# Performance work log

Measured on AMD Instinct MI355X. Metric: run time of the kernel, lower is better.

## Reference

```python
import jax, jax.numpy as jnp
import numpy as np

# dims: B batch, T seq, DM d_model, H kv heads, D head dim
B, T, DM = 4, 2048, 768
H, D = 4, 64          # n_kv_heads, d_head = d_model // n_heads = 768 // 12
DIM = H * D           # 256


def setup_inputs() -> dict:
    key = jax.random.key(0)
    kx, kq, kk, kv, ko, kg = jax.random.split(key, 6)
    s = 0.02  # init scale for weights
    return {
        "x": jax.random.normal(kx, (B, T, DM), jnp.float32),
        "Wq": jax.random.normal(kq, (DM, DIM), jnp.float32) * s,
        "Wk": jax.random.normal(kk, (DM, DIM), jnp.float32) * s,
        "Wv": jax.random.normal(kv, (DM, DIM), jnp.float32) * s,
        "Wo": jax.random.normal(ko, (DIM, DM), jnp.float32) * s,
        "Wg": jax.random.normal(kg, (DM, DM), jnp.float32) * s,
    }


def _feature_map(x):
    # F.elu(x) + 1.0  (strictly positive features)
    return jax.nn.elu(x) + 1.0


def reference(x, Wq, Wk, Wv, Wo, Wg):
    Bx, Tx, _ = x.shape
    q = _feature_map((x @ Wq).reshape(Bx, Tx, H, D))
    k = _feature_map((x @ Wk).reshape(Bx, Tx, H, D))
    v = (x @ Wv).reshape(Bx, Tx, H, D)

    # time-major for scan: [T, B, H, D]
    qT = q.transpose(1, 0, 2, 3)
    kT = k.transpose(1, 0, 2, 3)
    vT = v.transpose(1, 0, 2, 3)

    S0 = jnp.zeros((Bx, H, D, D), x.dtype)  # running sum of k v^T
    z0 = jnp.zeros((Bx, H, D), x.dtype)     # running sum of k

    def step(carry, inp):
        S, z = carry
        qi, ki, vi = inp  # each [B, H, D]
        S = S + ki[..., :, None] * vi[..., None, :]   # outer product update
        z = z + ki
        num = jnp.einsum('bhd,bhde->bhe', qi, S)
        den = jnp.maximum(jnp.sum(qi * z, axis=-1), 1e-6)  # clamp(min=1e-6)
        return (S, z), num / den[..., None]

    (_, _), outT = jax.lax.scan(step, (S0, z0), (qT, kT, vT))

    out = outT.transpose(1, 0, 2, 3).reshape(Bx, Tx, DIM)  # [B, T, H*D]
    gate = jax.nn.sigmoid(x @ Wg)
    return (out @ Wo) * gate
```

## Files before the change

kernel.cpp:

```cpp
#include <hip/hip_runtime.h>
#include <math.h>

typedef __attribute__((ext_vector_type(8))) short bf16x8;
typedef __attribute__((ext_vector_type(4))) float f32x4;

namespace {
constexpr int Bb  = 4;
constexpr int Tt  = 2048;
constexpr int DM  = 768;
constexpr int Hh  = 4;
constexpr int Dd  = 64;
constexpr int DIM = 256;
constexpr int BT  = Bb * Tt;
constexpr int CH  = 64;
constexpr int NC  = Tt / CH;
constexpr int NQKVG = 1536;
constexpr int MT  = BT / 128;
}

__device__ __forceinline__ float elu1(float x) { return x > 0.f ? x + 1.f : expf(x); }

__device__ __forceinline__ unsigned short f2bf(float f) {
  unsigned int x = __float_as_uint(f);
  unsigned int r = (x + 0x7fffu + ((x >> 16) & 1u)) >> 16;
  return (unsigned short)r;
}
__device__ __forceinline__ float bf2f(unsigned short u) {
  return __uint_as_float((unsigned int)u << 16);
}

__device__ __forceinline__ void gload16(const void* g, void* l) {
  __builtin_amdgcn_global_load_lds(
      (const __attribute__((address_space(1))) void*)g,
      (__attribute__((address_space(3))) void*)l, 16, 0, 0);
}

struct Stage32 {
  const short* a[2];
  const short* b[2];
  int seg;
  __device__ __forceinline__ void init(const short* Ag, size_t lda,
                                       const short* Bg, size_t ldb, int w, int l) {
    const int c16 = (l & 3) ^ ((l >> 3) & 3);
    seg = w * 2;
#pragma unroll
    for (int j = 0; j < 2; ++j) {
      int row = (seg + j) * 16 + (l >> 2);
      a[j] = Ag + (size_t)row * lda + c16 * 8;
      b[j] = Bg + (size_t)row * ldb + c16 * 8;
    }
  }
  __device__ __forceinline__ void issue(int k0, short* as, short* bs) const {
#pragma unroll
    for (int j = 0; j < 2; ++j) {
      gload16(a[j] + k0, (char*)as + (seg + j) * 1024);
      gload16(b[j] + k0, (char*)bs + (seg + j) * 1024);
    }
  }
};

__device__ __forceinline__ void xcd_tile(int bid, int& mt, int& nt) {
  int xcd = bid & 7;
  int idx = bid >> 3;
  mt = xcd * 8 + (idx & 7);
  nt = idx >> 3;
}

template <int NT>
__device__ __forceinline__ void kloop32(const Stage32& st, short* As0, short* As1,
                                        short* Bs0, short* Bs1,
                                        f32x4 (&acc)[4][4], int wr, int wc,
                                        int lr, int lg) {
  st.issue(0, As0, Bs0);
  st.issue(32, As1, Bs1);
#pragma unroll
  for (int t = 0; t < NT; ++t) {
    short* as = (t & 1) ? As1 : As0;
    short* bs = (t & 1) ? Bs1 : Bs0;
    if (t + 1 < NT)
      asm volatile("s_waitcnt vmcnt(4)" ::: "memory");
    else
      asm volatile("s_waitcnt vmcnt(0)" ::: "memory");
    __builtin_amdgcn_s_barrier();
    bf16x8 af[4], bf[4];
#pragma unroll
    for (int mi = 0; mi < 4; ++mi) {
      int r = wr * 64 + mi * 16 + lr;
      af[mi] = *(const bf16x8*)&as[r * 32 + (lg ^ ((r >> 1) & 3)) * 8];
    }
#pragma unroll
    for (int ni = 0; ni < 4; ++ni) {
      int r = wc * 64 + ni * 16 + lr;
      bf[ni] = *(const bf16x8*)&bs[r * 32 + (lg ^ ((r >> 1) & 3)) * 8];
    }
    asm volatile("s_waitcnt lgkmcnt(0)" ::: "memory");
    __builtin_amdgcn_sched_barrier(0);
    __builtin_amdgcn_s_barrier();
    if (t + 2 < NT) st.issue((t + 2) * 32, as, bs);
    __builtin_amdgcn_s_setprio(1);
#pragma unroll
    for (int mi = 0; mi < 4; ++mi)
#pragma unroll
      for (int ni = 0; ni < 4; ++ni)
        acc[mi][ni] = __builtin_amdgcn_mfma_f32_16x16x32_bf16(
            af[mi], bf[ni], acc[mi][ni], 0, 0, 0);
    __builtin_amdgcn_s_setprio(0);
  }
}

__global__ __launch_bounds__(256) void k_prep(
    const float* __restrict__ x, const float* __restrict__ Wq,
    const float* __restrict__ Wk, const float* __restrict__ Wv,
    const float* __restrict__ Wg, const float* __restrict__ Wo,
    unsigned short* __restrict__ xb, unsigned short* __restrict__ WT,
    unsigned short* __restrict__ WoT) {
  int bid = blockIdx.x;
  if (bid < 3072) {
    int i = bid * 256 + threadIdx.x;
    const float4* p = (const float4*)(x + (size_t)i * 8);
    float4 a = p[0], b = p[1];
    union { unsigned short u[8]; uint4 v; } r;
    r.u[0] = f2bf(a.x); r.u[1] = f2bf(a.y); r.u[2] = f2bf(a.z); r.u[3] = f2bf(a.w);
    r.u[4] = f2bf(b.x); r.u[5] = f2bf(b.y); r.u[6] = f2bf(b.z); r.u[7] = f2bf(b.w);
    *(uint4*)(xb + (size_t)i * 8) = r.v;
    return;
  }
  __shared__ float t[32][33];
  int idx = bid - 3072;
  const float* src;
  unsigned short* out;
  int K, N, n_off, ldo;
  if (idx < 576) {
    int z = idx / 192;
    idx %= 192;
    src = (z == 0) ? Wq : (z == 1) ? Wk : Wv;
    out = WT; K = 768; N = 256; n_off = z * 256; ldo = 768;
  } else if (idx < 1152) {
    idx -= 576;
    src = Wg; out = WT; K = 768; N = 768; n_off = 768; ldo = 768;
  } else {
    idx -= 1152;
    src = Wo; out = WoT; K = 256; N = 768; n_off = 0; ldo = 256;
  }
  int kt = idx % (K / 32), nt = idx / (K / 32);
  int k0 = kt * 32, n0 = nt * 32;
  const int tx = threadIdx.x & 31, ty = threadIdx.x >> 5;
  for (int i = ty; i < 32; i += 8)
    t[i][tx] = src[(size_t)(k0 + i) * N + n0 + tx];
  __syncthreads();
  for (int i = ty; i < 32; i += 8)
    out[(size_t)(n_off + n0 + i) * ldo + k0 + tx] = f2bf(t[tx][i]);
}

__global__ __launch_bounds__(256, 4) void k_gemm1(
    const unsigned short* __restrict__ xb, const unsigned short* __restrict__ WT,
    unsigned short* __restrict__ Q, unsigned short* __restrict__ K,
    unsigned short* __restrict__ V, unsigned short* __restrict__ G) {
  __shared__ __align__(16) char smem[32768];
  short* As0 = (short*)smem;
  short* As1 = (short*)(smem + 8192);
  short* Bs0 = (short*)(smem + 16384);
  short* Bs1 = (short*)(smem + 24576);
  const int tid = threadIdx.x;
  const int w = tid >> 6, l = tid & 63;
  const int lr = l & 15, lg = l >> 4;
  const int wr = w >> 1, wc = w & 1;
  int mt, nt;
  xcd_tile(blockIdx.x, mt, nt);
  const int m0 = mt * 128, n0 = nt * 128;

  Stage32 st;
  st.init((const short*)xb + (size_t)m0 * DM, DM,
          (const short*)WT + (size_t)n0 * DM, DM, w, l);

  f32x4 acc[4][4];
#pragma unroll
  for (int i = 0; i < 4; ++i)
#pragma unroll
    for (int j = 0; j < 4; ++j) acc[i][j] = (f32x4){0.f, 0.f, 0.f, 0.f};

  kloop32<DM / 32>(st, As0, As1, Bs0, Bs1, acc, wr, wc, lr, lg);
  __syncthreads();

  const int ttype = (n0 < 512) ? 0 : (n0 < 768) ? 1 : 2;
  unsigned short* Cs = (unsigned short*)smem;
#pragma unroll
  for (int mi = 0; mi < 4; ++mi)
#pragma unroll
    for (int ni = 0; ni < 4; ++ni)
#pragma unroll
      for (int r = 0; r < 4; ++r) {
        float v = acc[mi][ni][r];
        if (ttype == 0) v = elu1(v);
        else if (ttype == 2) v = 1.f / (1.f + expf(-v));
        Cs[(wr * 64 + mi * 16 + lg * 4 + r) * 128 + wc * 64 + ni * 16 + lr] =
            f2bf(v);
      }
  __syncthreads();
  unsigned short* dst;
  int ldd, cb;
  if (n0 < 256)      { dst = Q; ldd = DIM; cb = n0; }
  else if (n0 < 512) { dst = K; ldd = DIM; cb = n0 - 256; }
  else if (n0 < 768) { dst = V; ldd = DIM; cb = n0 - 512; }
  else               { dst = G; ldd = DM;  cb = n0 - 768; }
  const uint4* Cv = (const uint4*)Cs;
#pragma unroll
  for (int i = 0; i < 8; ++i) {
    int idx = tid + i * 256;
    int urow = idx >> 4, uc = idx & 15;
    *(uint4*)(dst + (size_t)(m0 + urow) * ldd + cb + uc * 8) = Cv[idx];
  }
}

__global__ __launch_bounds__(256) void k_chunksum(
    const unsigned short* __restrict__ K, const unsigned short* __restrict__ V,
    float* __restrict__ Sc, float* __restrict__ zc) {
  __shared__ float Ks[CH][68];
  __shared__ float Vs[CH][68];
  const int c = blockIdx.x, h = blockIdx.y, b = blockIdx.z;
  const int tx = threadIdx.x, ty = threadIdx.y;
  const int tid = ty * 16 + tx;
  const int t0 = c * CH;
#pragma unroll
  for (int l = 0; l < 4; ++l) {
    int idx = tid + l * 256;
    int d4 = idx & 15, t = idx >> 4;
    size_t o = (size_t)(b * Tt + t0 + t) * DIM + h * Dd + d4 * 4;
    short4 k4 = *(const short4*)(K + o);
    short4 v4 = *(const short4*)(V + o);
    Ks[t][d4 * 4 + 0] = bf2f(k4.x); Ks[t][d4 * 4 + 1] = bf2f(k4.y);
    Ks[t][d4 * 4 + 2] = bf2f(k4.z); Ks[t][d4 * 4 + 3] = bf2f(k4.w);
    Vs[t][d4 * 4 + 0] = bf2f(v4.x); Vs[t][d4 * 4 + 1] = bf2f(v4.y);
    Vs[t][d4 * 4 + 2] = bf2f(v4.z); Vs[t][d4 * 4 + 3] = bf2f(v4.w);
  }
  __syncthreads();
  float acc[4][4] = {};
  for (int t = 0; t < CH; ++t) {
    float4 k4 = *(const float4*)&Ks[t][ty * 4];
    float4 v4 = *(const float4*)&Vs[t][tx * 4];
    float kv[4] = {k4.x, k4.y, k4.z, k4.w};
    float vv[4] = {v4.x, v4.y, v4.z, v4.w};
#pragma unroll
    for (int i = 0; i < 4; ++i)
#pragma unroll
      for (int j = 0; j < 4; ++j) acc[i][j] += kv[i] * vv[j];
  }
  const size_t base = ((size_t)(b * Hh + h) * NC + c) * (Dd * Dd);
#pragma unroll
  for (int i = 0; i < 4; ++i) {
    float4 s4 = make_float4(acc[i][0], acc[i][1], acc[i][2], acc[i][3]);
    *(float4*)&Sc[base + (size_t)(ty * 4 + i) * Dd + tx * 4] = s4;
  }
  if (tid < Dd) {
    float s = 0.f;
    for (int t = 0; t < CH; ++t) s += Ks[t][tid];
    zc[((size_t)(b * Hh + h) * NC + c) * Dd + tid] = s;
  }
}

__global__ __launch_bounds__(256) void k_scan(float* __restrict__ Sc,
                                              float* __restrict__ zc) {
  const int bh = blockIdx.x;
  const int o = blockIdx.y * 256 + threadIdx.x;
  const size_t base = (size_t)bh * NC * (Dd * Dd) + o;
  float v[NC];
#pragma unroll
  for (int c = 0; c < NC; ++c) v[c] = Sc[base + (size_t)c * (Dd * Dd)];
  float run = 0.f;
#pragma unroll
  for (int c = 0; c < NC; ++c) {
    Sc[base + (size_t)c * (Dd * Dd)] = run;
    run += v[c];
  }
  if (blockIdx.y == 0 && threadIdx.x < Dd) {
    float rz = 0.f;
    for (int c = 0; c < NC; ++c) {
      size_t oz = ((size_t)bh * NC + c) * Dd + threadIdx.x;
      float cur = zc[oz];
      zc[oz] = rz;
      rz += cur;
    }
  }
}

__global__ __launch_bounds__(256) void k_out(
    const unsigned short* __restrict__ Q, const unsigned short* __restrict__ K,
    const unsigned short* __restrict__ V, const float* __restrict__ Sc,
    const float* __restrict__ zc, unsigned short* __restrict__ O) {
  __shared__ float Qs[CH][68];
  __shared__ float KVs[CH * 68];
  __shared__ float As[CH][68];
  __shared__ float Ss[Dd][68];
  __shared__ float zs[Dd];
  __shared__ float dens[CH];
  const int c = blockIdx.x, h = blockIdx.y, b = blockIdx.z;
  const int tx = threadIdx.x, ty = threadIdx.y;
  const int tid = ty * 16 + tx;
  const int t0 = c * CH;

#pragma unroll
  for (int l = 0; l < 4; ++l) {
    int idx = tid + l * 256;
    int d4 = idx & 15, t = idx >> 4;
    size_t o = (size_t)(b * Tt + t0 + t) * DIM + h * Dd + d4 * 4;
    short4 q4 = *(const short4*)(Q + o);
    short4 k4 = *(const short4*)(K + o);
    Qs[t][d4 * 4 + 0] = bf2f(q4.x); Qs[t][d4 * 4 + 1] = bf2f(q4.y);
    Qs[t][d4 * 4 + 2] = bf2f(q4.z); Qs[t][d4 * 4 + 3] = bf2f(q4.w);
    KVs[(d4 * 4 + 0) * 65 + t] = bf2f(k4.x);
    KVs[(d4 * 4 + 1) * 65 + t] = bf2f(k4.y);
    KVs[(d4 * 4 + 2) * 65 + t] = bf2f(k4.z);
    KVs[(d4 * 4 + 3) * 65 + t] = bf2f(k4.w);
  }
  __syncthreads();

  float acc[4][4] = {};
  for (int d0 = 0; d0 < Dd; d0 += 4) {
    float4 q4[4];
#pragma unroll
    for (int i = 0; i < 4; ++i) q4[i] = *(const float4*)&Qs[ty * 4 + i][d0];
#pragma unroll
    for (int dd = 0; dd < 4; ++dd) {
      int d = d0 + dd;
      float kv[4];
#pragma unroll
      for (int j = 0; j < 4; ++j) kv[j] = KVs[d * 65 + tx * 4 + j];
#pragma unroll
      for (int i = 0; i < 4; ++i) {
        float qv = ((const float*)&q4[i])[dd];
#pragma unroll
        for (int j = 0; j < 4; ++j) acc[i][j] += qv * kv[j];
      }
    }
  }
#pragma unroll
  for (int i = 0; i < 4; ++i)
#pragma unroll
    for (int j = 0; j < 4; ++j) {
      int ti = ty * 4 + i, sj = tx * 4 + j;
      As[ti][sj] = (sj <= ti) ? acc[i][j] : 0.f;
    }
  __syncthreads();

#pragma unroll
  for (int l = 0; l < 4; ++l) {
    int idx = tid + l * 256;
    int d4 = idx & 15, t = idx >> 4;
    size_t o = (size_t)(b * Tt + t0 + t) * DIM + h * Dd + d4 * 4;
    short4 v4 = *(const short4*)(V + o);
    KVs[t * 68 + d4 * 4 + 0] = bf2f(v4.x);
    KVs[t * 68 + d4 * 4 + 1] = bf2f(v4.y);
    KVs[t * 68 + d4 * 4 + 2] = bf2f(v4.z);
    KVs[t * 68 + d4 * 4 + 3] = bf2f(v4.w);
  }
  const size_t sbase = ((size_t)(b * Hh + h) * NC + c) * (Dd * Dd);
#pragma unroll
  for (int l = 0; l < 4; ++l) {
    int idx = tid + l * 256;
    int e4 = idx & 15, dd = idx >> 4;
    float4 s4 = *(const float4*)&Sc[sbase + (size_t)dd * Dd + e4 * 4];
    Ss[dd][e4 * 4 + 0] = s4.x; Ss[dd][e4 * 4 + 1] = s4.y;
    Ss[dd][e4 * 4 + 2] = s4.z; Ss[dd][e4 * 4 + 3] = s4.w;
  }
  if (tid < Dd) zs[tid] = zc[((size_t)(b * Hh + h) * NC + c) * Dd + tid];
  __syncthreads();

  if (tid < CH) {
    int i = tid;
    float rs = 0.f;
    for (int j = 0; j < CH; ++j) rs += As[i][j];
    float qz = 0.f;
    for (int d = 0; d < Dd; ++d) qz += Qs[i][d] * zs[d];
    dens[i] = fmaxf(rs + qz, 1e-6f);
  }
  float oacc[4][4] = {};
  for (int j = 0; j < CH; ++j) {
    float4 v4 = *(const float4*)&KVs[j * 68 + tx * 4];
    float vv[4] = {v4.x, v4.y, v4.z, v4.w};
    float av[4];
#pragma unroll
    for (int i = 0; i < 4; ++i) av[i] = As[ty * 4 + i][j];
#pragma unroll
    for (int i = 0; i < 4; ++i)
#pragma unroll
      for (int jj = 0; jj < 4; ++jj) oacc[i][jj] += av[i] * vv[jj];
  }
  for (int d = 0; d < Dd; ++d) {
    float4 s4 = *(const float4*)&Ss[d][tx * 4];
    float sv[4] = {s4.x, s4.y, s4.z, s4.w};
    float qv[4];
#pragma unroll
    for (int i = 0; i < 4; ++i) qv[i] = Qs[ty * 4 + i][d];
#pragma unroll
    for (int i = 0; i < 4; ++i)
#pragma unroll
      for (int jj = 0; jj < 4; ++jj) oacc[i][jj] += qv[i] * sv[jj];
  }
  __syncthreads();
#pragma unroll
  for (int i = 0; i < 4; ++i) {
    float inv = 1.f / dens[ty * 4 + i];
#pragma unroll
    for (int jj = 0; jj < 4; ++jj) {
      O[(size_t)(b * Tt + t0 + ty * 4 + i) * DIM + h * Dd + tx * 4 + jj] =
          f2bf(oacc[i][jj] * inv);
    }
  }
}

__global__ __launch_bounds__(256, 4) void k_gemm2(
    const unsigned short* __restrict__ Ob, const unsigned short* __restrict__ WoT,
    const unsigned short* __restrict__ G, float* __restrict__ out) {
  __shared__ __align__(16) char smem[32768];
  short* As0 = (short*)smem;
  short* As1 = (short*)(smem + 8192);
  short* Bs0 = (short*)(smem + 16384);
  short* Bs1 = (short*)(smem + 24576);
  const int tid = threadIdx.x;
  const int w = tid >> 6, l = tid & 63;
  const int lr = l & 15, lg = l >> 4;
  const int wr = w >> 1, wc = w & 1;
  int mt, nt;
  xcd_tile(blockIdx.x, mt, nt);
  const int m0 = mt * 128, n0 = nt * 128;

  Stage32 st;
  st.init((const short*)Ob + (size_t)m0 * DIM, DIM,
          (const short*)WoT + (size_t)n0 * DIM, DIM, w, l);

  f32x4 acc[4][4];
#pragma unroll
  for (int i = 0; i < 4; ++i)
#pragma unroll
    for (int j = 0; j < 4; ++j) acc[i][j] = (f32x4){0.f, 0.f, 0.f, 0.f};

  kloop32<DIM / 32>(st, As0, As1, Bs0, Bs1, acc, wr, wc, lr, lg);

  float* Cf = (float*)smem;
#pragma unroll
  for (int half = 0; half < 2; ++half) {
    __syncthreads();
    if (wr == half) {
#pragma unroll
      for (int mi = 0; mi < 4; ++mi)
#pragma unroll
        for (int ni = 0; ni < 4; ++ni)
#pragma unroll
          for (int r = 0; r < 4; ++r)
            Cf[(mi * 16 + lg * 4 + r) * 128 + wc * 64 + ni * 16 + lr] =
                acc[mi][ni][r];
    }
    __syncthreads();
    const float4* Cv = (const float4*)Cf;
#pragma unroll
    for (int i = 0; i < 8; ++i) {
      int idx = tid + i * 256;
      int urow = idx >> 5, uc = idx & 31;
      float4 cv = Cv[idx];
      size_t go = (size_t)(m0 + half * 64 + urow) * DM + n0 + uc * 4;
      short4 g4 = *(const short4*)(G + go);
      float4 ov;
      ov.x = cv.x * bf2f(g4.x);
      ov.y = cv.y * bf2f(g4.y);
      ov.z = cv.z * bf2f(g4.z);
      ov.w = cv.w * bf2f(g4.w);
      *(float4*)(out + go) = ov;
    }
  }
}

extern "C" void kernel_launch(void* const* d_in, const int* in_sizes, int n_in,
                              void* d_out, int out_size, void* d_ws,
                              size_t ws_size, hipStream_t stream) {
  const float* x  = (const float*)d_in[0];
  const float* Wq = (const float*)d_in[1];
  const float* Wk = (const float*)d_in[2];
  const float* Wv = (const float*)d_in[3];
  const float* Wo = (const float*)d_in[4];
  const float* Wg = (const float*)d_in[5];
  float* out = (float*)d_out;

  char* p = (char*)d_ws;
  size_t off = 0;
  auto alloc = [&](size_t bytes) {
    void* r = p + off;
    off = (off + bytes + 255) & ~(size_t)255;
    return r;
  };
  unsigned short* xb  = (unsigned short*)alloc((size_t)BT * DM * 2);
  unsigned short* WT  = (unsigned short*)alloc((size_t)NQKVG * DM * 2);
  unsigned short* WoT = (unsigned short*)alloc((size_t)DM * DIM * 2);
  unsigned short* Q   = (unsigned short*)alloc((size_t)BT * DIM * 2);
  unsigned short* Kf  = (unsigned short*)alloc((size_t)BT * DIM * 2);
  unsigned short* Vf  = (unsigned short*)alloc((size_t)BT * DIM * 2);
  unsigned short* G   = (unsigned short*)alloc((size_t)BT * DM * 2);
  unsigned short* Ob  = (unsigned short*)alloc((size_t)BT * DIM * 2);
  float* Sc = (float*)alloc((size_t)Bb * Hh * NC * Dd * Dd * 4);
  float* zc = (float*)alloc((size_t)Bb * Hh * NC * Dd * 4);

  k_prep<<<dim3(3072 + 1344), dim3(256), 0, stream>>>(x, Wq, Wk, Wv, Wg, Wo,
                                                      xb, WT, WoT);

  k_gemm1<<<dim3(MT * (NQKVG / 128)), dim3(256), 0, stream>>>(
      xb, WT, Q, Kf, Vf, G);

  dim3 blk(16, 16);
  k_chunksum<<<dim3(NC, Hh, Bb), blk, 0, stream>>>(Kf, Vf, Sc, zc);
  k_scan<<<dim3(Bb * Hh, Dd * Dd / 256), dim3(256), 0, stream>>>(Sc, zc);
  k_out<<<dim3(NC, Hh, Bb), blk, 0, stream>>>(Q, Kf, Vf, Sc, zc, Ob);

  k_gemm2<<<dim3(MT * (DM / 128)), dim3(256), 0, stream>>>(Ob, WoT, G, out);
}
```

Baseline: 86.45 us.

## Use bf16 MFMA for chunk state sums and intra-chunk attention output

Rewrites k_chunksum and k_out to keep K, V, Q and the chunk state as bf16 in swizzled shared memory and compute K^T V, Q K^T and the combined P V + Q S products with 16x16x32 bf16 MFMA instructions instead of scalar fp32 FMAs. The denominator is computed from MFMA accumulators with wave shuffles, and output is staged through shared memory for vectorised stores. The goal is to cut the ALU and LDS cost of the linear-attention chunk kernels. In exchange, the running state S and the masked scores are rounded to bf16 before the matmul, which loses some accuracy.

```diff
diff --git a/kernel.cpp b/kernel.cpp
--- a/kernel.cpp
+++ b/kernel.cpp
@@ -215,46 +215,74 @@
 __global__ __launch_bounds__(256) void k_chunksum(
     const unsigned short* __restrict__ K, const unsigned short* __restrict__ V,
     float* __restrict__ Sc, float* __restrict__ zc) {
-  __shared__ float Ks[CH][68];
-  __shared__ float Vs[CH][68];
+  __shared__ __align__(16) char smem[16384];
+  short* Kt = (short*)smem;
+  short* Vt = (short*)(smem + 8192);
   const int c = blockIdx.x, h = blockIdx.y, b = blockIdx.z;
-  const int tx = threadIdx.x, ty = threadIdx.y;
-  const int tid = ty * 16 + tx;
-  const int t0 = c * CH;
-#pragma unroll
-  for (int l = 0; l < 4; ++l) {
-    int idx = tid + l * 256;
-    int d4 = idx & 15, t = idx >> 4;
-    size_t o = (size_t)(b * Tt + t0 + t) * DIM + h * Dd + d4 * 4;
-    short4 k4 = *(const short4*)(K + o);
-    short4 v4 = *(const short4*)(V + o);
-    Ks[t][d4 * 4 + 0] = bf2f(k4.x); Ks[t][d4 * 4 + 1] = bf2f(k4.y);
-    Ks[t][d4 * 4 + 2] = bf2f(k4.z); Ks[t][d4 * 4 + 3] = bf2f(k4.w);
-    Vs[t][d4 * 4 + 0] = bf2f(v4.x); Vs[t][d4 * 4 + 1] = bf2f(v4.y);
-    Vs[t][d4 * 4 + 2] = bf2f(v4.z); Vs[t][d4 * 4 + 3] = bf2f(v4.w);
-  }
-  __syncthreads();
-  float acc[4][4] = {};
-  for (int t = 0; t < CH; ++t) {
-    float4 k4 = *(const float4*)&Ks[t][ty * 4];
-    float4 v4 = *(const float4*)&Vs[t][tx * 4];
-    float kv[4] = {k4.x, k4.y, k4.z, k4.w};
-    float vv[4] = {v4.x, v4.y, v4.z, v4.w};
-#pragma unroll
-    for (int i = 0; i < 4; ++i)
-#pragma unroll
-      for (int j = 0; j < 4; ++j) acc[i][j] += kv[i] * vv[j];
-  }
-  const size_t base = ((size_t)(b * Hh + h) * NC + c) * (Dd * Dd);
-#pragma unroll
-  for (int i = 0; i < 4; ++i) {
-    float4 s4 = make_float4(acc[i][0], acc[i][1], acc[i][2], acc[i][3]);
-    *(float4*)&Sc[base + (size_t)(ty * 4 + i) * Dd + tx * 4] = s4;
-  }
+  const int tid = threadIdx.x;
+  const int w = tid >> 6, l = tid & 63;
+  const int lr = l & 15, lg = l >> 4;
+  const size_t rowbase = ((size_t)(b * Tt + c * CH)) * DIM + h * Dd;
+
+#pragma unroll
+  for (int it = 0; it < 4; ++it) {
+    int idx = tid + it * 256;
+    int t = idx >> 4, d4 = idx & 15;
+    short4 k4 = *(const short4*)((const short*)K + rowbase + (size_t)t * DIM + d4 * 4);
+    short4 v4 = *(const short4*)((const short*)V + rowbase + (size_t)t * DIM + d4 * 4);
+    const short* kk = (const short*)&k4;
+    const short* vv = (const short*)&v4;
+#pragma unroll
+    for (int j = 0; j < 4; ++j) {
+      int e = d4 * 4 + j;
+      int sl = ((t >> 3) ^ (e & 7)) * 16 + (t & 7) * 2;
+      *(short*)((char*)Kt + e * 128 + sl) = kk[j];
+      *(short*)((char*)Vt + e * 128 + sl) = vv[j];
+    }
+  }
+  __syncthreads();
+
   if (tid < Dd) {
     float s = 0.f;
-    for (int t = 0; t < CH; ++t) s += Ks[t][tid];
+    for (int t = 0; t < CH; ++t) {
+      unsigned short u = *(const unsigned short*)(
+          (char*)Kt + tid * 128 + (((t >> 3) ^ (tid & 7)) * 16) + (t & 7) * 2);
+      s += bf2f(u);
+    }
     zc[((size_t)(b * Hh + h) * NC + c) * Dd + tid] = s;
+  }
+
+  f32x4 a[4];
+#pragma unroll
+  for (int nf = 0; nf < 4; ++nf) a[nf] = (f32x4){0.f, 0.f, 0.f, 0.f};
+  const int rd = w * 16 + lr;
+#pragma unroll
+  for (int ks = 0; ks < 2; ++ks) {
+    bf16x8 af = *(const bf16x8*)((char*)Kt + rd * 128 +
+                                 (((ks * 4 + lg) ^ (rd & 7)) * 16));
+#pragma unroll
+    for (int nf = 0; nf < 4; ++nf) {
+      int re = nf * 16 + lr;
+      bf16x8 bf = *(const bf16x8*)((char*)Vt + re * 128 +
+                                   (((ks * 4 + lg) ^ (re & 7)) * 16));
+      a[nf] = __builtin_amdgcn_mfma_f32_16x16x32_bf16(af, bf, a[nf], 0, 0, 0);
+    }
+  }
+  __syncthreads();
+
+  float* Cf = (float*)smem;
+#pragma unroll
+  for (int nf = 0; nf < 4; ++nf)
+#pragma unroll
+    for (int r = 0; r < 4; ++r)
+      Cf[(w * 16 + lg * 4 + r) * 64 + nf * 16 + lr] = a[nf][r];
+  __syncthreads();
+  const size_t base = ((size_t)(b * Hh + h) * NC + c) * (Dd * Dd);
+  const float4* Cv = (const float4*)Cf;
+#pragma unroll
+  for (int it = 0; it < 4; ++it) {
+    int idx = tid + it * 256;
+    *(float4*)&Sc[base + (size_t)idx * 4] = Cv[idx];
   }
 }
 
@@ -287,124 +315,140 @@
     const unsigned short* __restrict__ Q, const unsigned short* __restrict__ K,
     const unsigned short* __restrict__ V, const float* __restrict__ Sc,
     const float* __restrict__ zc, unsigned short* __restrict__ O) {
-  __shared__ float Qs[CH][68];
-  __shared__ float KVs[CH * 68];
-  __shared__ float As[CH][68];
-  __shared__ float Ss[Dd][68];
-  __shared__ float zs[Dd];
-  __shared__ float dens[CH];
+  __shared__ __align__(16) char smem[41216];
+  short* Qs = (short*)smem;
+  short* Ks = (short*)(smem + 8192);
+  short* Vt = (short*)(smem + 16384);
+  short* St = (short*)(smem + 24576);
+  short* Ps = (short*)(smem + 32768);
+  float* zs = (float*)(smem + 40960);
   const int c = blockIdx.x, h = blockIdx.y, b = blockIdx.z;
-  const int tx = threadIdx.x, ty = threadIdx.y;
-  const int tid = ty * 16 + tx;
-  const int t0 = c * CH;
-
-#pragma unroll
-  for (int l = 0; l < 4; ++l) {
-    int idx = tid + l * 256;
-    int d4 = idx & 15, t = idx >> 4;
-    size_t o = (size_t)(b * Tt + t0 + t) * DIM + h * Dd + d4 * 4;
-    short4 q4 = *(const short4*)(Q + o);
-    short4 k4 = *(const short4*)(K + o);
-    Qs[t][d4 * 4 + 0] = bf2f(q4.x); Qs[t][d4 * 4 + 1] = bf2f(q4.y);
-    Qs[t][d4 * 4 + 2] = bf2f(q4.z); Qs[t][d4 * 4 + 3] = bf2f(q4.w);
-    KVs[(d4 * 4 + 0) * 65 + t] = bf2f(k4.x);
-    KVs[(d4 * 4 + 1) * 65 + t] = bf2f(k4.y);
-    KVs[(d4 * 4 + 2) * 65 + t] = bf2f(k4.z);
-    KVs[(d4 * 4 + 3) * 65 + t] = bf2f(k4.w);
-  }
-  __syncthreads();
-
-  float acc[4][4] = {};
-  for (int d0 = 0; d0 < Dd; d0 += 4) {
-    float4 q4[4];
-#pragma unroll
-    for (int i = 0; i < 4; ++i) q4[i] = *(const float4*)&Qs[ty * 4 + i][d0];
-#pragma unroll
-    for (int dd = 0; dd < 4; ++dd) {
-      int d = d0 + dd;
-      float kv[4];
-#pragma unroll
-      for (int j = 0; j < 4; ++j) kv[j] = KVs[d * 65 + tx * 4 + j];
-#pragma unroll
-      for (int i = 0; i < 4; ++i) {
-        float qv = ((const float*)&q4[i])[dd];
-#pragma unroll
-        for (int j = 0; j < 4; ++j) acc[i][j] += qv * kv[j];
-      }
-    }
-  }
-#pragma unroll
-  for (int i = 0; i < 4; ++i)
+  const int tid = threadIdx.x;
+  const int w = tid >> 6, l = tid & 63;
+  const int lr = l & 15, lg = l >> 4;
+  const size_t rowbase = ((size_t)(b * Tt + c * CH)) * DIM + h * Dd;
+
+  {
+    const int c16 = (l & 7) ^ ((l >> 3) & 7);
+#pragma unroll
+    for (int i = 0; i < 2; ++i) {
+      int row = i * 32 + w * 8 + (l >> 3);
+      gload16((const short*)Q + rowbase + (size_t)row * DIM + c16 * 8,
+              (char*)Qs + (i * 32 + w * 8) * 128);
+      gload16((const short*)K + rowbase + (size_t)row * DIM + c16 * 8,
+              (char*)Ks + (i * 32 + w * 8) * 128);
+    }
+  }
+  const size_t sbase = ((size_t)(b * Hh + h) * NC + c) * (Dd * Dd);
+  if (tid < Dd) zs[tid] = zc[((size_t)(b * Hh + h) * NC + c) * Dd + tid];
+#pragma unroll
+  for (int it = 0; it < 4; ++it) {
+    int idx = tid + it * 256;
+    int t = idx >> 4, d4 = idx & 15;
+    short4 v4 = *(const short4*)((const short*)V + rowbase + (size_t)t * DIM + d4 * 4);
+    const short* vv = (const short*)&v4;
 #pragma unroll
     for (int j = 0; j < 4; ++j) {
-      int ti = ty * 4 + i, sj = tx * 4 + j;
-      As[ti][sj] = (sj <= ti) ? acc[i][j] : 0.f;
-    }
-  __syncthreads();
-
-#pragma unroll
-  for (int l = 0; l < 4; ++l) {
-    int idx = tid + l * 256;
-    int d4 = idx & 15, t = idx >> 4;
-    size_t o = (size_t)(b * Tt + t0 + t) * DIM + h * Dd + d4 * 4;
-    short4 v4 = *(const short4*)(V + o);
-    KVs[t * 68 + d4 * 4 + 0] = bf2f(v4.x);
-    KVs[t * 68 + d4 * 4 + 1] = bf2f(v4.y);
-    KVs[t * 68 + d4 * 4 + 2] = bf2f(v4.z);
-    KVs[t * 68 + d4 * 4 + 3] = bf2f(v4.w);
-  }
-  const size_t sbase = ((size_t)(b * Hh + h) * NC + c) * (Dd * Dd);
-#pragma unroll
-  for (int l = 0; l < 4; ++l) {
-    int idx = tid + l * 256;
-    int e4 = idx & 15, dd = idx >> 4;
-    float4 s4 = *(const float4*)&Sc[sbase + (size_t)dd * Dd + e4 * 4];
-    Ss[dd][e4 * 4 + 0] = s4.x; Ss[dd][e4 * 4 + 1] = s4.y;
-    Ss[dd][e4 * 4 + 2] = s4.z; Ss[dd][e4 * 4 + 3] = s4.w;
-  }
-  if (tid < Dd) zs[tid] = zc[((size_t)(b * Hh + h) * NC + c) * Dd + tid];
-  __syncthreads();
-
-  if (tid < CH) {
-    int i = tid;
-    float rs = 0.f;
-    for (int j = 0; j < CH; ++j) rs += As[i][j];
-    float qz = 0.f;
-    for (int d = 0; d < Dd; ++d) qz += Qs[i][d] * zs[d];
-    dens[i] = fmaxf(rs + qz, 1e-6f);
-  }
-  float oacc[4][4] = {};
-  for (int j = 0; j < CH; ++j) {
-    float4 v4 = *(const float4*)&KVs[j * 68 + tx * 4];
-    float vv[4] = {v4.x, v4.y, v4.z, v4.w};
-    float av[4];
-#pragma unroll
-    for (int i = 0; i < 4; ++i) av[i] = As[ty * 4 + i][j];
-#pragma unroll
-    for (int i = 0; i < 4; ++i)
-#pragma unroll
-      for (int jj = 0; jj < 4; ++jj) oacc[i][jj] += av[i] * vv[jj];
-  }
-  for (int d = 0; d < Dd; ++d) {
-    float4 s4 = *(const float4*)&Ss[d][tx * 4];
-    float sv[4] = {s4.x, s4.y, s4.z, s4.w};
-    float qv[4];
-#pragma unroll
-    for (int i = 0; i < 4; ++i) qv[i] = Qs[ty * 4 + i][d];
-#pragma unroll
-    for (int i = 0; i < 4; ++i)
-#pragma unroll
-      for (int jj = 0; jj < 4; ++jj) oacc[i][jj] += qv[i] * sv[jj];
-  }
-  __syncthreads();
-#pragma unroll
-  for (int i = 0; i < 4; ++i) {
-    float inv = 1.f / dens[ty * 4 + i];
-#pragma unroll
-    for (int jj = 0; jj < 4; ++jj) {
-      O[(size_t)(b * Tt + t0 + ty * 4 + i) * DIM + h * Dd + tx * 4 + jj] =
-          f2bf(oacc[i][jj] * inv);
-    }
+      int e = d4 * 4 + j;
+      *(short*)((char*)Vt + e * 128 + (((t >> 3) ^ (e & 7)) * 16) + (t & 7) * 2) = vv[j];
+    }
+    float4 s4 = *(const float4*)&Sc[sbase + (size_t)t * 64 + d4 * 4];
+    const float* sv = (const float*)&s4;
+#pragma unroll
+    for (int j = 0; j < 4; ++j) {
+      int e = d4 * 4 + j;
+      *(short*)((char*)St + e * 128 + (((t >> 3) ^ (e & 7)) * 16) + (t & 7) * 2) =
+          (short)f2bf(sv[j]);
+    }
+  }
+  __syncthreads();
+
+  f32x4 a0[4];
+#pragma unroll
+  for (int nf = 0; nf < 4; ++nf) a0[nf] = (f32x4){0.f, 0.f, 0.f, 0.f};
+  const int rq = w * 16 + lr;
+#pragma unroll
+  for (int ks = 0; ks < 2; ++ks) {
+    bf16x8 af = *(const bf16x8*)((char*)Qs + rq * 128 +
+                                 (((ks * 4 + lg) ^ (rq & 7)) * 16));
+#pragma unroll
+    for (int nf = 0; nf < 4; ++nf) {
+      int rk = nf * 16 + lr;
+      bf16x8 bf = *(const bf16x8*)((char*)Ks + rk * 128 +
+                                   (((ks * 4 + lg) ^ (rk & 7)) * 16));
+      a0[nf] = __builtin_amdgcn_mfma_f32_16x16x32_bf16(af, bf, a0[nf], 0, 0, 0);
+    }
+  }
+
+  float part[4] = {0.f, 0.f, 0.f, 0.f};
+#pragma unroll
+  for (int nf = 0; nf < 4; ++nf) {
+    int col = nf * 16 + lr;
+#pragma unroll
+    for (int r = 0; r < 4; ++r) {
+      int row = w * 16 + lg * 4 + r;
+      float av = (col <= row) ? a0[nf][r] : 0.f;
+      part[r] += av;
+      *(short*)((char*)Ps + row * 128 +
+                ((((nf * 2) + (lr >> 3)) ^ (row & 7)) * 16) + (lr & 7) * 2) =
+          (short)f2bf(av);
+    }
+  }
+#pragma unroll
+  for (int r = 0; r < 4; ++r) {
+    int row = w * 16 + lg * 4 + r;
+#pragma unroll
+    for (int j = 0; j < 4; ++j) {
+      int d = lr + j * 16;
+      unsigned short qu = *(const unsigned short*)(
+          (char*)Qs + row * 128 + (((d >> 3) ^ (row & 7)) * 16) + (d & 7) * 2);
+      part[r] += bf2f(qu) * zs[d];
+    }
+  }
+  float inv[4];
+#pragma unroll
+  for (int r = 0; r < 4; ++r) {
+    float s = part[r];
+    s += __shfl_xor(s, 1);
+    s += __shfl_xor(s, 2);
+    s += __shfl_xor(s, 4);
+    s += __shfl_xor(s, 8);
+    inv[r] = 1.f / fmaxf(s, 1e-6f);
+  }
+  __syncthreads();
+
+  f32x4 a1[4];
+#pragma unroll
+  for (int nf = 0; nf < 4; ++nf) a1[nf] = (f32x4){0.f, 0.f, 0.f, 0.f};
+#pragma unroll
+  for (int ks = 0; ks < 4; ++ks) {
+    const char* abase = (ks < 2) ? (const char*)Ps : (const char*)Qs;
+    const char* bbase = (ks < 2) ? (const char*)Vt : (const char*)St;
+    int kslot = (ks & 1) * 4 + lg;
+    bf16x8 af = *(const bf16x8*)(abase + rq * 128 + ((kslot ^ (rq & 7)) * 16));
+#pragma unroll
+    for (int nf = 0; nf < 4; ++nf) {
+      int re = nf * 16 + lr;
+      bf16x8 bf = *(const bf16x8*)(bbase + re * 128 + ((kslot ^ (re & 7)) * 16));
+      a1[nf] = __builtin_amdgcn_mfma_f32_16x16x32_bf16(af, bf, a1[nf], 0, 0, 0);
+    }
+  }
+  __syncthreads();
+
+#pragma unroll
+  for (int nf = 0; nf < 4; ++nf)
+#pragma unroll
+    for (int r = 0; r < 4; ++r) {
+      int row = w * 16 + lg * 4 + r;
+      Ps[row * 64 + nf * 16 + lr] = (short)f2bf(a1[nf][r] * inv[r]);
+    }
+  __syncthreads();
+  const uint4* Pv = (const uint4*)Ps;
+#pragma unroll
+  for (int i = 0; i < 2; ++i) {
+    int idx = tid + i * 256;
+    int row = idx >> 3, uc = idx & 7;
+    *(uint4*)((unsigned short*)O + rowbase + (size_t)row * DIM + uc * 8) = Pv[idx];
   }
 }
 
@@ -504,10 +548,9 @@
   k_gemm1<<<dim3(MT * (NQKVG / 128)), dim3(256), 0, stream>>>(
       xb, WT, Q, Kf, Vf, G);
 
-  dim3 blk(16, 16);
-  k_chunksum<<<dim3(NC, Hh, Bb), blk, 0, stream>>>(Kf, Vf, Sc, zc);
+  k_chunksum<<<dim3(NC, Hh, Bb), dim3(256), 0, stream>>>(Kf, Vf, Sc, zc);
   k_scan<<<dim3(Bb * Hh, Dd * Dd / 256), dim3(256), 0, stream>>>(Sc, zc);
-  k_out<<<dim3(NC, Hh, Bb), blk, 0, stream>>>(Q, Kf, Vf, Sc, zc, Ob);
+  k_out<<<dim3(NC, Hh, Bb), dim3(256), 0, stream>>>(Q, Kf, Vf, Sc, zc, Ob);
 
   k_gemm2<<<dim3(MT * (DM / 128)), dim3(256), 0, stream>>>(Ob, WoT, G, out);
 }
```

New measurement: 76.95 us. -11.0%, faster.
